# Optimization experiments

Measured on AMD Instinct MI355X. Metric: run time of the kernel, lower is better.

Reference implementation:

```python
import jax, jax.numpy as jnp
import numpy as np

I, T, Q, K, E, H = 16, 64, 196, 32, 512, 8
D = E // H


def setup_inputs() -> dict:
    key = jax.random.key(0)
    ks = jax.random.split(key, 8)
    image = jax.random.normal(ks[0], (I, Q, E), dtype=jnp.float32)
    text = jax.random.normal(ks[1], (T, K, E), dtype=jnp.float32)
    text_mask = jax.random.randint(ks[2], (T, K), 0, 2).astype(bool)
    text_mask = text_mask.at[:, 0].set(True)  # avoid fully-masked rows
    s = 1.0 / np.sqrt(D)
    Wq = jax.random.normal(ks[3], (D, D), dtype=jnp.float32) * s
    Wk = jax.random.normal(ks[4], (D, D), dtype=jnp.float32) * s
    Wv = jax.random.normal(ks[5], (D, D), dtype=jnp.float32) * s
    Wo = jax.random.normal(ks[6], (E, E), dtype=jnp.float32) * (1.0 / np.sqrt(E))
    bo = jnp.zeros((E,), dtype=jnp.float32)
    return {"image": image, "text": text, "text_mask": text_mask,
            "Wq": Wq, "Wk": Wk, "Wv": Wv, "Wo": Wo, "bo": bo}


def reference(image, text, text_mask, Wq, Wk, Wv, Wo, bo):
    i, q_len, e = image.shape
    t, k_len, _ = text.shape
    img = image.reshape(i, q_len, H, D)   # i q h d
    txt = text.reshape(t, k_len, H, D)    # t k h d
    # torch Linear: x @ W.T (bias=False for q/k/v)
    query = jnp.einsum('iqhd,ed->iqhe', img, Wq)
    key_p = jnp.einsum('tkhd,ed->tkhe', txt, Wk)
    value = jnp.einsum('tkhd,ed->tkhe', txt, Wv)
    energy = jnp.einsum('tkhd,iqhd->ithqk', key_p, query)
    neg = jnp.finfo(jnp.float32).min
    energy = jnp.where(text_mask[None, :, None, None, :], energy, neg)
    scaled = energy / (e ** 0.5)
    attention = jax.nn.softmax(scaled, axis=-1)        # over k
    text_attention = jax.nn.softmax(scaled, axis=-2)   # over q
    out = jnp.einsum('ithqk,tkhd->itqhd', attention, value)
    out = out.reshape(i, t, q_len, e)                  # i t q (h d)
    out = jnp.einsum('itqe,fe->itqf', out, Wo) + bo    # fc_out
    out = out.mean(axis=2)                             # pooling_type='mean'
    return out, attention, text_attention
```

## Files before the change

### kernel.cpp

```cpp
#include <hip/hip_runtime.h>
#include <math.h>

#define I_N 16
#define T_N 64
#define Q_N 196
#define K_N 32
#define E_N 512
#define H_N 8
#define D_N 64

#define NEG_MASKED (-1.5038454e37f)
#define INV_SQRT_E (0.044194173824159216f)

typedef __attribute__((ext_vector_type(8))) short bf16x8;
typedef __attribute__((ext_vector_type(4))) float f32x4;

__device__ __forceinline__ short f2bf(float x) {
    unsigned u = __builtin_bit_cast(unsigned, x);
    unsigned r = (u + 0x7fffu + ((u >> 16) & 1u)) >> 16;
    return (short)r;
}
__device__ __forceinline__ float bf2f(short s) {
    unsigned u = ((unsigned)(unsigned short)s) << 16;
    return __builtin_bit_cast(float, u);
}

__global__ __launch_bounds__(512) void detect_mask_kernel(const unsigned int* __restrict__ mask,
                                                          int* __restrict__ flag) {
    __shared__ int notSimple, sawFloat;
    int tid = threadIdx.x;
    if (tid == 0) { notSimple = 0; sawFloat = 0; }
    __syncthreads();
    unsigned int v = mask[tid];
    if (v != 0u && v != 1u && v != 0x3f800000u) atomicOr(&notSimple, 1);
    if (v == 0x3f800000u) atomicOr(&sawFloat, 1);
    __syncthreads();
    if (tid == 0) flag[0] = notSimple ? 2 : (sawFloat ? 1 : 0);
}

__global__ __launch_bounds__(256) void proj_q_kernel(const float* __restrict__ x,
                                                     const float* __restrict__ W,
                                                     unsigned short* __restrict__ qh,
                                                     unsigned short* __restrict__ ql) {
    __shared__ float sWt[64 * 65];
    __shared__ float sX[16 * 64];
    int tid = threadIdx.x;
    for (int j = tid; j < 4096; j += 256) {
        int n = j >> 6, d = j & 63;
        sWt[d * 65 + n] = W[j];
    }
    int rowBase = blockIdx.x * 16;
    for (int j = tid; j < 1024; j += 256) sX[j] = x[rowBase * 64 + j];
    __syncthreads();
    int wave = tid >> 6, lane = tid & 63;
    float acc[4] = {0.f, 0.f, 0.f, 0.f};
    for (int d = 0; d < 64; ++d) {
        float w = sWt[d * 65 + lane];
#pragma unroll
        for (int j = 0; j < 4; ++j) acc[j] += sX[(wave * 4 + j) * 64 + d] * w;
    }
#pragma unroll
    for (int j = 0; j < 4; ++j) {
        int r = rowBase + wave * 4 + j;
        int i = r / (Q_N * H_N);
        int rem = r - i * (Q_N * H_N);
        int q = rem >> 3, h = rem & 7;
        size_t dst = (((size_t)i * H_N + h) * Q_N + q) * 64 + lane;
        float a = acc[j] * INV_SQRT_E;
        short hi = f2bf(a);
        qh[dst] = (unsigned short)hi;
        ql[dst] = (unsigned short)f2bf(a - bf2f(hi));
    }
}

__global__ __launch_bounds__(256) void proj_kv_kernel(const float* __restrict__ x,
                                                      const float* __restrict__ Wk,
                                                      const float* __restrict__ Wv,
                                                      unsigned short* __restrict__ kh,
                                                      unsigned short* __restrict__ kl,
                                                      float* __restrict__ vout) {
    __shared__ float sWkT[64 * 65];
    __shared__ float sWvT[64 * 65];
    __shared__ float sX[16 * 64];
    int tid = threadIdx.x;
    for (int j = tid; j < 4096; j += 256) {
        int n = j >> 6, d = j & 63;
        sWkT[d * 65 + n] = Wk[j];
        sWvT[d * 65 + n] = Wv[j];
    }
    int rowBase = blockIdx.x * 16;
    for (int j = tid; j < 1024; j += 256) sX[j] = x[rowBase * 64 + j];
    __syncthreads();
    int wave = tid >> 6, lane = tid & 63;
    float ak[4] = {0.f, 0.f, 0.f, 0.f};
    float av[4] = {0.f, 0.f, 0.f, 0.f};
    for (int d = 0; d < 64; ++d) {
        float wk = sWkT[d * 65 + lane];
        float wv = sWvT[d * 65 + lane];
#pragma unroll
        for (int j = 0; j < 4; ++j) {
            float xv = sX[(wave * 4 + j) * 64 + d];
            ak[j] += xv * wk;
            av[j] += xv * wv;
        }
    }
#pragma unroll
    for (int j = 0; j < 4; ++j) {
        int r = rowBase + wave * 4 + j;
        int t = r >> 8;
        int rem = r & 255;
        int k = rem >> 3, h = rem & 7;
        size_t dst = (((size_t)t * H_N + h) * K_N + k) * 64 + lane;
        short hi = f2bf(ak[j]);
        kh[dst] = (unsigned short)hi;
        kl[dst] = (unsigned short)f2bf(ak[j] - bf2f(hi));
        vout[dst] = av[j];
    }
}

__global__ __launch_bounds__(256) void transpose_wo_kernel(const float* __restrict__ Wo,
                                                           float* __restrict__ WoT) {
    __shared__ float tile[32][33];
    int tx = threadIdx.x & 31, ty = threadIdx.x >> 5;
    int e0 = blockIdx.x * 32, f0 = blockIdx.y * 32;
#pragma unroll
    for (int k = 0; k < 4; ++k) {
        int fy = ty + k * 8;
        tile[fy][tx] = Wo[(size_t)(f0 + fy) * E_N + e0 + tx];
    }
    __syncthreads();
#pragma unroll
    for (int k = 0; k < 4; ++k) {
        int ey = ty + k * 8;
        WoT[(size_t)(e0 + ey) * E_N + f0 + tx] = tile[tx][ey];
    }
}

__global__ __launch_bounds__(256) void attn_kernel(const unsigned short* __restrict__ qhi,
                                                   const unsigned short* __restrict__ qlo,
                                                   const unsigned short* __restrict__ khi,
                                                   const unsigned short* __restrict__ klo,
                                                   const float* __restrict__ vproj,
                                                   const int* __restrict__ mask,
                                                   const int* __restrict__ modeFlag,
                                                   float* __restrict__ attn_out,
                                                   float* __restrict__ tattn_out,
                                                   float* __restrict__ pooled) {
    __shared__ float sS[Q_N * 33];
    __shared__ float sMrow[Q_N];
    __shared__ float sRrow[Q_N];
    __shared__ float sColRed[4 * 32];
    __shared__ float sColRed2[8 * 32];
    __shared__ float sColRed3[8 * 32];
    __shared__ float sColMax[32];
    __shared__ float sColR[32];
    __shared__ float sCa[32];
    __shared__ float sMask[K_N];

    int tid = threadIdx.x;
    int bid = blockIdx.x;
    int h = bid & 7;
    int t = (bid >> 3) & 63;
    int i = bid >> 9;
    int lane = tid & 63, wave = tid >> 6;
    int quad = lane >> 4, lid = lane & 15;

    int mode = modeFlag[0];
    if (tid < K_N) {
        int idx = t * K_N + tid;
        bool keep;
        if (mode == 2)      keep = ((const unsigned char*)mask)[idx] != 0;
        else if (mode == 1) keep = ((const float*)mask)[idx] != 0.0f;
        else                keep = mask[idx] != 0;
        sMask[tid] = keep ? 1.0f : 0.0f;
    }
    __syncthreads();

    size_t kbase = ((size_t)t * H_N + h) * (K_N * 64);
    bf16x8 Bh[2][2], Bl[2][2];
#pragma unroll
    for (int nt = 0; nt < 2; ++nt)
#pragma unroll
        for (int ks = 0; ks < 2; ++ks) {
            size_t off = kbase + (size_t)(nt * 16 + lid) * 64 + ks * 32 + quad * 8;
            Bh[nt][ks] = *(const bf16x8*)(khi + off);
            Bl[nt][ks] = *(const bf16x8*)(klo + off);
        }

    float keep0 = sMask[lid], keep1 = sMask[16 + lid];
    size_t qoff = ((size_t)i * H_N + h) * (Q_N * 64);

    float cm0 = -INFINITY, cm1 = -INFINITY;

    for (int mt = wave; mt < 13; mt += 4) {
        int qb = mt * 16;
        int qr = qb + lid; if (qr > Q_N - 1) qr = Q_N - 1;
        const unsigned short* ph = qhi + qoff + (size_t)qr * 64 + quad * 8;
        const unsigned short* pl = qlo + qoff + (size_t)qr * 64 + quad * 8;
        bf16x8 Ah0 = *(const bf16x8*)ph;
        bf16x8 Ah1 = *(const bf16x8*)(ph + 32);
        bf16x8 Al0 = *(const bf16x8*)pl;
        bf16x8 Al1 = *(const bf16x8*)(pl + 32);

        f32x4 acc0 = {0.f, 0.f, 0.f, 0.f}, acc1 = {0.f, 0.f, 0.f, 0.f};
        acc0 = __builtin_amdgcn_mfma_f32_16x16x32_bf16(Al0, Bh[0][0], acc0, 0, 0, 0);
        acc0 = __builtin_amdgcn_mfma_f32_16x16x32_bf16(Ah0, Bl[0][0], acc0, 0, 0, 0);
        acc0 = __builtin_amdgcn_mfma_f32_16x16x32_bf16(Ah0, Bh[0][0], acc0, 0, 0, 0);
        acc0 = __builtin_amdgcn_mfma_f32_16x16x32_bf16(Al1, Bh[0][1], acc0, 0, 0, 0);
        acc0 = __builtin_amdgcn_mfma_f32_16x16x32_bf16(Ah1, Bl[0][1], acc0, 0, 0, 0);
        acc0 = __builtin_amdgcn_mfma_f32_16x16x32_bf16(Ah1, Bh[0][1], acc0, 0, 0, 0);
        acc1 = __builtin_amdgcn_mfma_f32_16x16x32_bf16(Al0, Bh[1][0], acc1, 0, 0, 0);
        acc1 = __builtin_amdgcn_mfma_f32_16x16x32_bf16(Ah0, Bl[1][0], acc1, 0, 0, 0);
        acc1 = __builtin_amdgcn_mfma_f32_16x16x32_bf16(Ah0, Bh[1][0], acc1, 0, 0, 0);
        acc1 = __builtin_amdgcn_mfma_f32_16x16x32_bf16(Al1, Bh[1][1], acc1, 0, 0, 0);
        acc1 = __builtin_amdgcn_mfma_f32_16x16x32_bf16(Ah1, Bl[1][1], acc1, 0, 0, 0);
        acc1 = __builtin_amdgcn_mfma_f32_16x16x32_bf16(Ah1, Bh[1][1], acc1, 0, 0, 0);

#pragma unroll
        for (int reg = 0; reg < 4; ++reg) {
            int q = qb + quad * 4 + reg;
            if (q < Q_N) {
                float s0 = keep0 != 0.f ? acc0[reg] : NEG_MASKED;
                float s1 = keep1 != 0.f ? acc1[reg] : NEG_MASKED;
                sS[q * 33 + lid] = s0;
                sS[q * 33 + 16 + lid] = s1;
                cm0 = fmaxf(cm0, s0);
                cm1 = fmaxf(cm1, s1);
            }
        }
    }
    cm0 = fmaxf(cm0, __shfl_xor(cm0, 16));
    cm0 = fmaxf(cm0, __shfl_xor(cm0, 32));
    cm1 = fmaxf(cm1, __shfl_xor(cm1, 16));
    cm1 = fmaxf(cm1, __shfl_xor(cm1, 32));
    if (lane < 16) {
        sColRed[wave * 32 + lid] = cm0;
        sColRed[wave * 32 + 16 + lid] = cm1;
    }
    __syncthreads();

    if (tid < 32) {
        float m = fmaxf(fmaxf(sColRed[tid], sColRed[32 + tid]),
                        fmaxf(sColRed[64 + tid], sColRed[96 + tid]));
        sColMax[tid] = m;
    }
    if (tid < Q_N) {
        const float* r = &sS[tid * 33];
        float rv[32];
#pragma unroll
        for (int k = 0; k < 32; ++k) rv[k] = r[k];
#pragma unroll
        for (int k = 0; k < 16; ++k) rv[k] = fmaxf(rv[k], rv[k + 16]);
#pragma unroll
        for (int k = 0; k < 8; ++k) rv[k] = fmaxf(rv[k], rv[k + 8]);
        float m = fmaxf(fmaxf(fmaxf(rv[0], rv[1]), fmaxf(rv[2], rv[3])),
                        fmaxf(fmaxf(rv[4], rv[5]), fmaxf(rv[6], rv[7])));
        float s = 0.f;
#pragma unroll
        for (int k = 0; k < 32; ++k) s += __expf(r[k] - m);
        sMrow[tid] = m;
        sRrow[tid] = 1.0f / s;
    }
    __syncthreads();

    int kc = tid & 31, sub = tid >> 5;
    {
        float mcol = sColMax[kc];
        float cs = 0.f, ca = 0.f;
        for (int qq = sub; qq < Q_N; qq += 8) {
            float v = sS[qq * 33 + kc];
            cs += __expf(v - mcol);
            ca += __expf(v - sMrow[qq]) * sRrow[qq];
        }
        sColRed2[sub * 32 + kc] = cs;
        sColRed3[sub * 32 + kc] = ca;
    }
    __syncthreads();
    if (tid < 32) {
        float s1 = 0.f, s2 = 0.f;
#pragma unroll
        for (int s = 0; s < 8; ++s) {
            s1 += sColRed2[s * 32 + tid];
            s2 += sColRed3[s * 32 + tid];
        }
        sColR[tid] = 1.0f / s1;
        sCa[tid] = s2;
    }
    __syncthreads();

    {
        float* ab = attn_out + (size_t)bid * (Q_N * K_N);
        float* tb = tattn_out + (size_t)bid * (Q_N * K_N);
        for (int j = tid; j < Q_N * K_N; j += 256) {
            int qq = j >> 5, k = j & 31;
            float v = sS[qq * 33 + k];
            float a = __expf(v - sMrow[qq]) * sRrow[qq];
            float ta = __expf(v - sColMax[k]) * sColR[k];
            __builtin_nontemporal_store(a, ab + j);
            __builtin_nontemporal_store(ta, tb + j);
        }
    }

    if (tid < 64) {
        const float* vb = vproj + kbase + tid;
        float acc = 0.f;
#pragma unroll
        for (int k = 0; k < K_N; ++k) acc += sCa[k] * vb[k * 64];
        pooled[((size_t)(i * T_N + t)) * E_N + h * 64 + tid] = acc;
    }
}

__global__ __launch_bounds__(256) void fc_out_kernel(const float* __restrict__ pooled,
                                                     const float* __restrict__ WoT,
                                                     const float* __restrict__ bo,
                                                     float* __restrict__ out) {
    __shared__ float sPT[E_N * 4];
    int tid = threadIdx.x;
    int p0 = blockIdx.x * 4;
#pragma unroll
    for (int j = 0; j < 4; ++j) {
        sPT[tid * 4 + j] = pooled[(size_t)(p0 + j) * E_N + tid];
        sPT[(256 + tid) * 4 + j] = pooled[(size_t)(p0 + j) * E_N + 256 + tid];
    }
    __syncthreads();
    const float4* sPT4 = (const float4*)sPT;
    int f = blockIdx.y * 256 + tid;
    float4 acc = make_float4(0.f, 0.f, 0.f, 0.f);
    for (int e = 0; e < E_N; e += 2) {
        float w0 = WoT[(size_t)e * E_N + f];
        float w1 = WoT[(size_t)(e + 1) * E_N + f];
        float4 pv0 = sPT4[e];
        float4 pv1 = sPT4[e + 1];
        acc.x += pv0.x * w0 + pv1.x * w1;
        acc.y += pv0.y * w0 + pv1.y * w1;
        acc.z += pv0.z * w0 + pv1.z * w1;
        acc.w += pv0.w * w0 + pv1.w * w1;
    }
    const float invQ = 1.0f / 196.0f;
    float b = bo[f];
    out[(size_t)(p0 + 0) * E_N + f] = b + acc.x * invQ;
    out[(size_t)(p0 + 1) * E_N + f] = b + acc.y * invQ;
    out[(size_t)(p0 + 2) * E_N + f] = b + acc.z * invQ;
    out[(size_t)(p0 + 3) * E_N + f] = b + acc.w * invQ;
}

extern "C" void kernel_launch(void* const* d_in, const int* in_sizes, int n_in,
                              void* d_out, int out_size, void* d_ws, size_t ws_size,
                              hipStream_t stream) {
    const float* image = (const float*)d_in[0];
    const float* text  = (const float*)d_in[1];
    const int*   mask  = (const int*)d_in[2];
    const float* Wq    = (const float*)d_in[3];
    const float* Wk    = (const float*)d_in[4];
    const float* Wv    = (const float*)d_in[5];
    const float* Wo    = (const float*)d_in[6];
    const float* bo    = (const float*)d_in[7];
    float* out = (float*)d_out;

    unsigned short* qhi = (unsigned short*)d_ws;
    unsigned short* qlo = qhi + (size_t)I_N * Q_N * H_N * D_N;
    unsigned short* khi = qlo + (size_t)I_N * Q_N * H_N * D_N;
    unsigned short* klo = khi + (size_t)T_N * K_N * H_N * D_N;
    float* vproj  = (float*)(klo + (size_t)T_N * K_N * H_N * D_N);
    float* pooled = vproj + (size_t)T_N * K_N * H_N * D_N;
    float* WoT    = pooled + (size_t)I_N * T_N * E_N;
    int*   mode   = (int*)(WoT + (size_t)E_N * E_N);

    float* attn  = out + (size_t)I_N * T_N * E_N;
    float* tattn = attn + (size_t)I_N * T_N * H_N * Q_N * K_N;

    detect_mask_kernel<<<1, 512, 0, stream>>>((const unsigned int*)mask, mode);
    proj_q_kernel<<<(I_N * Q_N * H_N) / 16, 256, 0, stream>>>(image, Wq, qhi, qlo);
    proj_kv_kernel<<<(T_N * K_N * H_N) / 16, 256, 0, stream>>>(text, Wk, Wv, khi, klo, vproj);
    transpose_wo_kernel<<<dim3(16, 16), 256, 0, stream>>>(Wo, WoT);
    attn_kernel<<<I_N * T_N * H_N, 256, 0, stream>>>(qhi, qlo, khi, klo, vproj, mask, mode,
                                                     attn, tattn, pooled);
    fc_out_kernel<<<dim3((I_N * T_N) / 4, 2), 256, 0, stream>>>(pooled, WoT, bo, out);
}
```

Baseline: 510.9 us.

## Fuse column softmax sum into score pass and vectorize attention output stores

The column (over-q) softmax denominator is now computed with an online max/sum rescaling during the MFMA score loop and merged across lanes and waves, which removes the separate column-sum pass over shared memory. The column-attention accumulation for pooling is folded into the output-writing loop, which now has each thread handle four consecutive k values and write 16-byte nontemporal vector stores. This drops two block barriers and one full sweep of the score tile. In exchange, each score element costs two extra exps, and the final per-column sums come from shuffle and cross-wave reductions.

Result: no change. 500.9 us (-1.9%).

```diff
diff --git a/kernel.cpp b/kernel.cpp
--- a/kernel.cpp
+++ b/kernel.cpp
@@ -149,9 +149,9 @@
     __shared__ float sS[Q_N * 33];
     __shared__ float sMrow[Q_N];
     __shared__ float sRrow[Q_N];
-    __shared__ float sColRed[4 * 32];
-    __shared__ float sColRed2[8 * 32];
-    __shared__ float sColRed3[8 * 32];
+    __shared__ float sColM[4 * 32];
+    __shared__ float sColS[4 * 32];
+    __shared__ float sCaW[4 * 32];
     __shared__ float sColMax[32];
     __shared__ float sColR[32];
     __shared__ float sCa[32];
@@ -190,7 +190,7 @@
     float keep0 = sMask[lid], keep1 = sMask[16 + lid];
     size_t qoff = ((size_t)i * H_N + h) * (Q_N * 64);
 
-    float cm0 = -INFINITY, cm1 = -INFINITY;
+    float cm0 = -INFINITY, cs0 = 0.f, cm1 = -INFINITY, cs1 = 0.f;
 
     for (int mt = wave; mt < 13; mt += 4) {
         int qb = mt * 16;
@@ -224,25 +224,42 @@
                 float s1 = keep1 != 0.f ? acc1[reg] : NEG_MASKED;
                 sS[q * 33 + lid] = s0;
                 sS[q * 33 + 16 + lid] = s1;
-                cm0 = fmaxf(cm0, s0);
-                cm1 = fmaxf(cm1, s1);
+                float nm0 = fmaxf(cm0, s0);
+                cs0 = cs0 * __expf(cm0 - nm0) + __expf(s0 - nm0);
+                cm0 = nm0;
+                float nm1 = fmaxf(cm1, s1);
+                cs1 = cs1 * __expf(cm1 - nm1) + __expf(s1 - nm1);
+                cm1 = nm1;
             }
         }
     }
-    cm0 = fmaxf(cm0, __shfl_xor(cm0, 16));
-    cm0 = fmaxf(cm0, __shfl_xor(cm0, 32));
-    cm1 = fmaxf(cm1, __shfl_xor(cm1, 16));
-    cm1 = fmaxf(cm1, __shfl_xor(cm1, 32));
+#pragma unroll
+    for (int d = 16; d <= 32; d <<= 1) {
+        float om = __shfl_xor(cm0, d), os = __shfl_xor(cs0, d);
+        float nm = fmaxf(cm0, om);
+        cs0 = cs0 * __expf(cm0 - nm) + os * __expf(om - nm);
+        cm0 = nm;
+        om = __shfl_xor(cm1, d); os = __shfl_xor(cs1, d);
+        nm = fmaxf(cm1, om);
+        cs1 = cs1 * __expf(cm1 - nm) + os * __expf(om - nm);
+        cm1 = nm;
+    }
     if (lane < 16) {
-        sColRed[wave * 32 + lid] = cm0;
-        sColRed[wave * 32 + 16 + lid] = cm1;
+        sColM[wave * 32 + lid] = cm0;
+        sColS[wave * 32 + lid] = cs0;
+        sColM[wave * 32 + 16 + lid] = cm1;
+        sColS[wave * 32 + 16 + lid] = cs1;
     }
     __syncthreads();
 
     if (tid < 32) {
-        float m = fmaxf(fmaxf(sColRed[tid], sColRed[32 + tid]),
-                        fmaxf(sColRed[64 + tid], sColRed[96 + tid]));
+        float m0 = sColM[tid], m1 = sColM[32 + tid];
+        float m2 = sColM[64 + tid], m3 = sColM[96 + tid];
+        float m = fmaxf(fmaxf(m0, m1), fmaxf(m2, m3));
+        float s = sColS[tid] * __expf(m0 - m) + sColS[32 + tid] * __expf(m1 - m) +
+                  sColS[64 + tid] * __expf(m2 - m) + sColS[96 + tid] * __expf(m3 - m);
         sColMax[tid] = m;
+        sColR[tid] = 1.0f / s;
     }
     if (tid < Q_N) {
         const float* r = &sS[tid * 33];
@@ -263,43 +280,48 @@
     }
     __syncthreads();
 
-    int kc = tid & 31, sub = tid >> 5;
-    {
-        float mcol = sColMax[kc];
-        float cs = 0.f, ca = 0.f;
-        for (int qq = sub; qq < Q_N; qq += 8) {
-            float v = sS[qq * 33 + kc];
-            cs += __expf(v - mcol);
-            ca += __expf(v - sMrow[qq]) * sRrow[qq];
+    int rowt = tid >> 3, kg = tid & 7;
+    float mc[4], cr[4];
+#pragma unroll
+    for (int c = 0; c < 4; ++c) {
+        mc[c] = sColMax[kg * 4 + c];
+        cr[c] = sColR[kg * 4 + c];
+    }
+    float ca[4] = {0.f, 0.f, 0.f, 0.f};
+    float* ab = attn_out + (size_t)bid * (Q_N * K_N);
+    float* tb = tattn_out + (size_t)bid * (Q_N * K_N);
+#pragma unroll
+    for (int j = 0; j < 7; ++j) {
+        int qq = rowt + 32 * j;
+        if (qq < Q_N) {
+            float mr = sMrow[qq], rr = sRrow[qq];
+            const float* rp = &sS[qq * 33 + kg * 4];
+            float v0 = rp[0], v1 = rp[1], v2 = rp[2], v3 = rp[3];
+            float e0 = __expf(v0 - mr), e1 = __expf(v1 - mr);
+            float e2 = __expf(v2 - mr), e3 = __expf(v3 - mr);
+            f32x4 av = {e0 * rr, e1 * rr, e2 * rr, e3 * rr};
+            ca[0] += av[0]; ca[1] += av[1]; ca[2] += av[2]; ca[3] += av[3];
+            f32x4 tv = {__expf(v0 - mc[0]) * cr[0],
+                        __expf(v1 - mc[1]) * cr[1],
+                        __expf(v2 - mc[2]) * cr[2],
+                        __expf(v3 - mc[3]) * cr[3]};
+            __builtin_nontemporal_store(av, (f32x4*)(ab + qq * 32 + kg * 4));
+            __builtin_nontemporal_store(tv, (f32x4*)(tb + qq * 32 + kg * 4));
         }
-        sColRed2[sub * 32 + kc] = cs;
-        sColRed3[sub * 32 + kc] = ca;
-    }
-    __syncthreads();
-    if (tid < 32) {
-        float s1 = 0.f, s2 = 0.f;
-#pragma unroll
-        for (int s = 0; s < 8; ++s) {
-            s1 += sColRed2[s * 32 + tid];
-            s2 += sColRed3[s * 32 + tid];
-        }
-        sColR[tid] = 1.0f / s1;
-        sCa[tid] = s2;
-    }
-    __syncthreads();
-
-    {
-        float* ab = attn_out + (size_t)bid * (Q_N * K_N);
-        float* tb = tattn_out + (size_t)bid * (Q_N * K_N);
-        for (int j = tid; j < Q_N * K_N; j += 256) {
-            int qq = j >> 5, k = j & 31;
-            float v = sS[qq * 33 + k];
-            float a = __expf(v - sMrow[qq]) * sRrow[qq];
-            float ta = __expf(v - sColMax[k]) * sColR[k];
-            __builtin_nontemporal_store(a, ab + j);
-            __builtin_nontemporal_store(ta, tb + j);
-        }
-    }
+    }
+#pragma unroll
+    for (int c = 0; c < 4; ++c) {
+        ca[c] += __shfl_xor(ca[c], 8);
+        ca[c] += __shfl_xor(ca[c], 16);
+        ca[c] += __shfl_xor(ca[c], 32);
+    }
+    if (lane < 8) {
+#pragma unroll
+        for (int c = 0; c < 4; ++c) sCaW[wave * 32 + lane * 4 + c] = ca[c];
+    }
+    __syncthreads();
+    if (tid < 32) sCa[tid] = sCaW[tid] + sCaW[32 + tid] + sCaW[64 + tid] + sCaW[96 + tid];
+    __syncthreads();
 
     if (tid < 64) {
         const float* vb = vproj + kbase + tid;
```
